# Kernel tuning notes

Hardware: AMD Instinct MI355X
Metric: run time of the kernel (lower is better)

The kernel has to match this reference:

```python
import jax, jax.numpy as jnp
import numpy as np

B, T, D, O, E = 4, 4096, 256, 256, 16


def setup_inputs() -> dict:
    key = jax.random.key(0)
    ks = jax.random.split(key, 5)
    s_in = 1.0 / np.sqrt(D)
    x = jax.random.normal(ks[0], (B, T, D), dtype=jnp.float32)
    We = jax.random.uniform(ks[1], (E, D, O), minval=-s_in, maxval=s_in, dtype=jnp.float32)
    be = jax.random.uniform(ks[2], (E, O), minval=-s_in, maxval=s_in, dtype=jnp.float32)
    Wg = jax.random.uniform(ks[3], (D, E), minval=-s_in, maxval=s_in, dtype=jnp.float32)
    bg = jax.random.uniform(ks[4], (E,), minval=-s_in, maxval=s_in, dtype=jnp.float32)
    return {"x": x, "We": We, "be": be, "Wg": Wg, "bg": bg}


def reference(x, We, be, Wg, bg):
    # gate: softmax over experts  [B,T,E]
    gate = jax.nn.softmax(jnp.einsum("btd,de->bte", x, Wg) + bg, axis=-1)
    # all experts: batched GEMM  [B,T,E,O]
    h = jax.nn.gelu(jnp.einsum("btd,edo->bteo", x, We) + be, approximate=False)
    # softmax-weighted sum over experts  [B,T,O]
    return jnp.einsum("bteo,bte->bto", h, gate)
```

## Files before the change

### kernel.cpp

```cpp
#include <hip/hip_runtime.h>
#include <stdint.h>

#define KD 256
#define NO 256
#define NE 16
#define BM 64
#define BN 128
#define XROW 264
#define GROW 68

typedef short bf16x8 __attribute__((ext_vector_type(8)));
typedef float f32x4 __attribute__((ext_vector_type(4)));

__device__ __forceinline__ unsigned short f2bf(float f) {
  uint32_t u = __float_as_uint(f);
  u += 0x7fffu + ((u >> 16) & 1u);
  return (unsigned short)(u >> 16);
}
__device__ __forceinline__ float bf2f(unsigned short h) {
  return __uint_as_float(((uint32_t)h) << 16);
}
__device__ __forceinline__ float gelu_f(float h) {
#if __has_builtin(__builtin_amdgcn_exp2f)
  float zn = h * fmaf(-0.10294817f, h * h, -2.3022077f);
  return h * __builtin_amdgcn_rcpf(1.0f + __builtin_amdgcn_exp2f(zn));
#else
  float z = h * fmaf(0.07135481627f, h * h, 1.5957691216f);
  return h * __builtin_amdgcn_rcpf(1.0f + __expf(-z));
#endif
}

__global__ void moe_prep(const float* __restrict__ We, unsigned short* __restrict__ Wf,
                         const float* __restrict__ Wg, unsigned short* __restrict__ Wgt)
{
  __shared__ float ts[256 * 17];
  const int tid = threadIdx.x;
  const int bid = blockIdx.x;
  if (bid < 256) {
    const int e = bid >> 4, ob = bid & 15;
    const float* src = We + (size_t)e * KD * NO + ob * 16;
    const int o = tid & 15, dg = tid >> 4;
#pragma unroll
    for (int p = 0; p < 16; ++p) {
      int d = p * 16 + dg;
      ts[d * 17 + o] = src[(size_t)d * NO + o];
    }
    __syncthreads();
    const int w = tid >> 6, l = tid & 63;
    const int q = l >> 4, ln = l & 15;
#pragma unroll
    for (int kk = 0; kk < 2; ++kk) {
      int kc = w + kk * 4;
      unsigned int pk[4];
#pragma unroll
      for (int h = 0; h < 4; ++h) {
        unsigned short lo = f2bf(ts[(kc * 32 + q * 8 + h * 2 + 0) * 17 + ln]);
        unsigned short hi = f2bf(ts[(kc * 32 + q * 8 + h * 2 + 1) * 17 + ln]);
        pk[h] = (unsigned int)lo | ((unsigned int)hi << 16);
      }
      uint4* dst = (uint4*)(Wf + ((((size_t)(e * 8 + kc) * 16 + ob) * 64) + l) * 8);
      *dst = make_uint4(pk[0], pk[1], pk[2], pk[3]);
    }
  } else {
    int d = tid;
    const float* wr = Wg + (size_t)d * NE;
#pragma unroll
    for (int e = 0; e < NE; ++e)
      Wgt[e * KD + d] = f2bf(wr[e]);
  }
}

__launch_bounds__(256, 2)
__global__ void moe_main(const float* __restrict__ x,
                         const uint4* __restrict__ Wf,
                         const unsigned short* __restrict__ Wgt,
                         const float* __restrict__ be,
                         const float* __restrict__ bg,
                         float* __restrict__ out)
{
  __shared__ __align__(16) unsigned short Xs[BM * XROW];
  __shared__ __align__(16) float gate_t[NE * GROW];
  __shared__ unsigned short be_h[NE * BN];

  const int tid = threadIdx.x;
  const int bid = blockIdx.x;
  const int half = bid & 1;
  const int n0 = half * BN;
  const int m0 = (bid >> 1) * BM;
  const int w = tid >> 6, lane = tid & 63;
  const int ln = lane & 15, quad = lane >> 4;
  const int eoff = __builtin_amdgcn_readfirstlane(((tid >> 6) * 4 + bid) & 15);

  const int voff = (half * 8 + w * 2) * 64 + lane;

  {
    const float4* xg = (const float4*)x + (size_t)m0 * (KD / 4);
#pragma unroll
    for (int p = 0; p < 16; ++p) {
      int idx = p * 256 + tid;
      int r = idx >> 6, c = idx & 63;
      float4 v = xg[r * (KD / 4) + c];
      uint32_t lo = (uint32_t)f2bf(v.x) | ((uint32_t)f2bf(v.y) << 16);
      uint32_t hi = (uint32_t)f2bf(v.z) | ((uint32_t)f2bf(v.w) << 16);
      *(uint2*)&Xs[r * XROW + c * 4] = make_uint2(lo, hi);
    }
  }
  uint4 b[4][2];
#pragma unroll
  for (int kc = 0; kc < 4; ++kc) {
    const uint4* p = Wf + ((size_t)eoff * 8 + kc) * 1024 + voff;
    b[kc][0] = p[0]; b[kc][1] = p[64];
  }
#pragma unroll
  for (int p = 0; p < 8; ++p) {
    int idx = p * 256 + tid;
    int e = idx >> 7, c = idx & 127;
    be_h[e * BN + c] = f2bf(be[e * NO + n0 + c]);
  }
  __syncthreads();

  bf16x8 a[4][8];
#pragma unroll
  for (int i = 0; i < 4; ++i)
#pragma unroll
    for (int kc = 0; kc < 8; ++kc)
      a[i][kc] = *(const bf16x8*)&Xs[(i * 16 + ln) * XROW + kc * 32 + quad * 8];

  {
    f32x4 g = {0.f, 0.f, 0.f, 0.f};
#pragma unroll
    for (int kc = 0; kc < 8; ++kc) {
      bf16x8 af = *(const bf16x8*)&Xs[(w * 16 + ln) * XROW + kc * 32 + quad * 8];
      bf16x8 wb = *(const bf16x8*)(Wgt + (size_t)ln * KD + kc * 32 + quad * 8);
      g = __builtin_amdgcn_mfma_f32_16x16x32_bf16(af, wb, g, 0, 0, 0);
    }
    float bgl = bg[ln];
#pragma unroll
    for (int r = 0; r < 4; ++r) {
      float v = g[r] + bgl;
      float mx = v;
#pragma unroll
      for (int msk = 1; msk < 16; msk <<= 1)
        mx = fmaxf(mx, __shfl_xor(mx, msk, 64));
      float ev = __expf(v - mx);
      float s = ev;
#pragma unroll
      for (int msk = 1; msk < 16; msk <<= 1)
        s += __shfl_xor(s, msk, 64);
      gate_t[ln * GROW + w * 16 + quad * 4 + r] = ev * __builtin_amdgcn_rcpf(s);
    }
  }
  __syncthreads();

  f32x4 acc[4][2], oacc[4][2];
#pragma unroll
  for (int i = 0; i < 4; ++i)
#pragma unroll
    for (int j = 0; j < 2; ++j) {
      acc[i][j] = (f32x4){0.f, 0.f, 0.f, 0.f};
      oacc[i][j] = (f32x4){0.f, 0.f, 0.f, 0.f};
    }

#pragma unroll 1
  for (int ei = 0; ei < NE; ++ei) {
    const int e  = (eoff + ei) & 15;
    const int en = (eoff + ei + 1) & 15;
    const uint4* bse = Wf + (size_t)e  * 8192 + voff;
    const uint4* bsn = Wf + (size_t)en * 8192 + voff;

#pragma unroll
    for (int kc = 0; kc < 8; ++kc) {
      uint4* bc = b[kc & 3];
#pragma unroll
      for (int i = 0; i < 4; ++i)
#pragma unroll
        for (int j = 0; j < 2; ++j)
          acc[i][j] = __builtin_amdgcn_mfma_f32_16x16x32_bf16(
              a[i][kc], *(const bf16x8*)&bc[j], acc[i][j], 0, 0, 0);
      if (kc < 4) {
        const uint4* p = bse + (kc + 4) * 1024;
        bc[0] = p[0]; bc[1] = p[64];
      } else if (ei < NE - 1) {
        const uint4* p = bsn + (kc - 4) * 1024;
        bc[0] = p[0]; bc[1] = p[64];
      }
    }
    {
      f32x4 gv[4];
#pragma unroll
      for (int i = 0; i < 4; ++i)
        gv[i] = *(const f32x4*)&gate_t[e * GROW + i * 16 + quad * 4];
      const float bb0 = bf2f(be_h[e * BN + w * 32 + ln]);
      const float bb1 = bf2f(be_h[e * BN + w * 32 + 16 + ln]);
#pragma unroll
      for (int i = 0; i < 4; ++i)
#pragma unroll
        for (int j = 0; j < 2; ++j)
#pragma unroll
          for (int r = 0; r < 4; ++r) {
            float hh = acc[i][j][r] + (j ? bb1 : bb0);
            oacc[i][j][r] = fmaf(gv[i][r], gelu_f(hh), oacc[i][j][r]);
            acc[i][j][r] = 0.f;
          }
    }
  }

#pragma unroll
  for (int i = 0; i < 4; ++i)
#pragma unroll
    for (int r = 0; r < 4; ++r) {
      int row = m0 + i * 16 + quad * 4 + r;
      float* orow = out + (size_t)row * NO + n0 + w * 32 + ln;
      orow[0]  = oacc[i][0][r];
      orow[16] = oacc[i][1][r];
    }
}

extern "C" void kernel_launch(void* const* d_in, const int* in_sizes, int n_in,
                              void* d_out, int out_size, void* d_ws, size_t ws_size,
                              hipStream_t stream) {
  const float* x  = (const float*)d_in[0];
  const float* We = (const float*)d_in[1];
  const float* be = (const float*)d_in[2];
  const float* Wg = (const float*)d_in[3];
  const float* bg = (const float*)d_in[4];
  float* out = (float*)d_out;
  unsigned short* Wf  = (unsigned short*)d_ws;
  unsigned short* Wgt = (unsigned short*)((char*)d_ws + (size_t)NE * NO * KD * 2);

  moe_prep<<<257, 256, 0, stream>>>(We, Wf, Wg, Wgt);
  moe_main<<<512, 256, 0, stream>>>(x, (const uint4*)Wf, Wgt, be, bg, out);
}
```

Measured before the change: 122.0 us.

## Move output accumulators to LDS and prefetch a whole expert's weights

The per-thread output accumulators move from registers into a shared-memory array, which frees registers. Those registers now hold all eight K-chunks of the next expert's weight fragments, so the whole next expert is prefetched during the current expert's MFMAs instead of half at a time. The prep kernel is split across twice as many blocks, each transposing half of the K dimension. The cost is extra LDS read-modify-write traffic every expert, 32KB more shared memory per block that may limit occupancy, and more register pressure from the larger weight buffer.

```diff
diff --git a/kernel.cpp b/kernel.cpp
--- a/kernel.cpp
+++ b/kernel.cpp
@@ -33,34 +33,31 @@
 __global__ void moe_prep(const float* __restrict__ We, unsigned short* __restrict__ Wf,
                          const float* __restrict__ Wg, unsigned short* __restrict__ Wgt)
 {
-  __shared__ float ts[256 * 17];
+  __shared__ float ts[128 * 17];
   const int tid = threadIdx.x;
   const int bid = blockIdx.x;
-  if (bid < 256) {
-    const int e = bid >> 4, ob = bid & 15;
-    const float* src = We + (size_t)e * KD * NO + ob * 16;
+  if (bid < 512) {
+    const int e = bid >> 5, ob = (bid >> 1) & 15, dh = bid & 1;
+    const float* src = We + ((size_t)e * KD + dh * 128) * NO + ob * 16;
     const int o = tid & 15, dg = tid >> 4;
 #pragma unroll
-    for (int p = 0; p < 16; ++p) {
+    for (int p = 0; p < 8; ++p) {
       int d = p * 16 + dg;
       ts[d * 17 + o] = src[(size_t)d * NO + o];
     }
     __syncthreads();
     const int w = tid >> 6, l = tid & 63;
     const int q = l >> 4, ln = l & 15;
-#pragma unroll
-    for (int kk = 0; kk < 2; ++kk) {
-      int kc = w + kk * 4;
-      unsigned int pk[4];
-#pragma unroll
-      for (int h = 0; h < 4; ++h) {
-        unsigned short lo = f2bf(ts[(kc * 32 + q * 8 + h * 2 + 0) * 17 + ln]);
-        unsigned short hi = f2bf(ts[(kc * 32 + q * 8 + h * 2 + 1) * 17 + ln]);
-        pk[h] = (unsigned int)lo | ((unsigned int)hi << 16);
-      }
-      uint4* dst = (uint4*)(Wf + ((((size_t)(e * 8 + kc) * 16 + ob) * 64) + l) * 8);
-      *dst = make_uint4(pk[0], pk[1], pk[2], pk[3]);
-    }
+    const int kc = dh * 4 + w;
+    unsigned int pk[4];
+#pragma unroll
+    for (int h = 0; h < 4; ++h) {
+      unsigned short lo = f2bf(ts[(w * 32 + q * 8 + h * 2 + 0) * 17 + ln]);
+      unsigned short hi = f2bf(ts[(w * 32 + q * 8 + h * 2 + 1) * 17 + ln]);
+      pk[h] = (unsigned int)lo | ((unsigned int)hi << 16);
+    }
+    uint4* dst = (uint4*)(Wf + ((((size_t)(e * 8 + kc) * 16 + ob) * 64) + l) * 8);
+    *dst = make_uint4(pk[0], pk[1], pk[2], pk[3]);
   } else {
     int d = tid;
     const float* wr = Wg + (size_t)d * NE;
@@ -81,6 +78,7 @@
   __shared__ __align__(16) unsigned short Xs[BM * XROW];
   __shared__ __align__(16) float gate_t[NE * GROW];
   __shared__ unsigned short be_h[NE * BN];
+  __shared__ __align__(16) f32x4 oaccL[8 * 256];
 
   const int tid = threadIdx.x;
   const int bid = blockIdx.x;
@@ -105,9 +103,9 @@
       *(uint2*)&Xs[r * XROW + c * 4] = make_uint2(lo, hi);
     }
   }
-  uint4 b[4][2];
-#pragma unroll
-  for (int kc = 0; kc < 4; ++kc) {
+  uint4 b[8][2];
+#pragma unroll
+  for (int kc = 0; kc < 8; ++kc) {
     const uint4* p = Wf + ((size_t)eoff * 8 + kc) * 1024 + voff;
     b[kc][0] = p[0]; b[kc][1] = p[64];
   }
@@ -127,6 +125,13 @@
       a[i][kc] = *(const bf16x8*)&Xs[(i * 16 + ln) * XROW + kc * 32 + quad * 8];
 
   {
+    const f32x4 z = (f32x4){0.f, 0.f, 0.f, 0.f};
+#pragma unroll
+    for (int q = 0; q < 8; ++q)
+      oaccL[q * 256 + tid] = z;
+  }
+
+  {
     f32x4 g = {0.f, 0.f, 0.f, 0.f};
 #pragma unroll
     for (int kc = 0; kc < 8; ++kc) {
@@ -152,36 +157,30 @@
   }
   __syncthreads();
 
-  f32x4 acc[4][2], oacc[4][2];
+  f32x4 acc[4][2];
 #pragma unroll
   for (int i = 0; i < 4; ++i)
 #pragma unroll
-    for (int j = 0; j < 2; ++j) {
+    for (int j = 0; j < 2; ++j)
       acc[i][j] = (f32x4){0.f, 0.f, 0.f, 0.f};
-      oacc[i][j] = (f32x4){0.f, 0.f, 0.f, 0.f};
-    }
 
 #pragma unroll 1
   for (int ei = 0; ei < NE; ++ei) {
     const int e  = (eoff + ei) & 15;
     const int en = (eoff + ei + 1) & 15;
-    const uint4* bse = Wf + (size_t)e  * 8192 + voff;
     const uint4* bsn = Wf + (size_t)en * 8192 + voff;
 
 #pragma unroll
     for (int kc = 0; kc < 8; ++kc) {
-      uint4* bc = b[kc & 3];
+      uint4* bc = b[kc];
 #pragma unroll
       for (int i = 0; i < 4; ++i)
 #pragma unroll
         for (int j = 0; j < 2; ++j)
           acc[i][j] = __builtin_amdgcn_mfma_f32_16x16x32_bf16(
               a[i][kc], *(const bf16x8*)&bc[j], acc[i][j], 0, 0, 0);
-      if (kc < 4) {
-        const uint4* p = bse + (kc + 4) * 1024;
-        bc[0] = p[0]; bc[1] = p[64];
-      } else if (ei < NE - 1) {
-        const uint4* p = bsn + (kc - 4) * 1024;
+      if (ei < NE - 1) {
+        const uint4* p = bsn + kc * 1024;
         bc[0] = p[0]; bc[1] = p[64];
       }
     }
@@ -195,25 +194,33 @@
 #pragma unroll
       for (int i = 0; i < 4; ++i)
 #pragma unroll
-        for (int j = 0; j < 2; ++j)
+        for (int j = 0; j < 2; ++j) {
+          const int q = i * 2 + j;
+          f32x4 prev = oaccL[q * 256 + tid];
+          const float bb = j ? bb1 : bb0;
 #pragma unroll
           for (int r = 0; r < 4; ++r) {
-            float hh = acc[i][j][r] + (j ? bb1 : bb0);
-            oacc[i][j][r] = fmaf(gv[i][r], gelu_f(hh), oacc[i][j][r]);
+            float hh = acc[i][j][r] + bb;
+            prev[r] = fmaf(gv[i][r], gelu_f(hh), prev[r]);
             acc[i][j][r] = 0.f;
           }
-    }
-  }
-
-#pragma unroll
-  for (int i = 0; i < 4; ++i)
+          oaccL[q * 256 + tid] = prev;
+        }
+    }
+  }
+
+#pragma unroll
+  for (int i = 0; i < 4; ++i) {
+    f32x4 o0 = oaccL[(i * 2 + 0) * 256 + tid];
+    f32x4 o1 = oaccL[(i * 2 + 1) * 256 + tid];
 #pragma unroll
     for (int r = 0; r < 4; ++r) {
       int row = m0 + i * 16 + quad * 4 + r;
       float* orow = out + (size_t)row * NO + n0 + w * 32 + ln;
-      orow[0]  = oacc[i][0][r];
-      orow[16] = oacc[i][1][r];
-    }
+      orow[0]  = o0[r];
+      orow[16] = o1[r];
+    }
+  }
 }
 
 extern "C" void kernel_launch(void* const* d_in, const int* in_sizes, int n_in,
@@ -228,6 +235,6 @@
   unsigned short* Wf  = (unsigned short*)d_ws;
   unsigned short* Wgt = (unsigned short*)((char*)d_ws + (size_t)NE * NO * KD * 2);
 
-  moe_prep<<<257, 256, 0, stream>>>(We, Wf, Wg, Wgt);
+  moe_prep<<<513, 256, 0, stream>>>(We, Wf, Wg, Wgt);
   moe_main<<<512, 256, 0, stream>>>(x, (const uint4*)Wf, Wgt, be, bg, out);
 }
```

Measured after the change: 139.1 us. 1.14x slower.
